# Kernel tuning notes

Hardware: AMD Instinct MI355X
Metric: run time of the kernel (lower is better)

Reference implementation:

```python
import jax, jax.numpy as jnp
import numpy as np

B, S, D, H = 8, 1024, 1024, 16
DH = D // H
EPS = 1e-5


def _layernorm(x):
    # elementwise_affine=False LayerNorm, eps=1e-5
    m = jnp.mean(x, axis=-1, keepdims=True)
    v = jnp.var(x, axis=-1, keepdims=True)
    return (x - m) * jax.lax.rsqrt(v + EPS)


def setup_inputs() -> dict:
    key = jax.random.key(0)
    ks = jax.random.split(key, 11)
    s = 0.02
    return {
        "x": jax.random.normal(ks[0], (B, S, D), jnp.float32),
        "y": jax.random.normal(ks[1], (B, 1, D), jnp.float32),
        "w_adaln": jax.random.normal(ks[2], (6 * D, D), jnp.float32) * s,
        "b_adaln": jnp.zeros((6 * D,), jnp.float32),
        "w_qkv": jax.random.normal(ks[3], (3 * D, D), jnp.float32) * s,
        "w_proj": jax.random.normal(ks[4], (D, D), jnp.float32) * s,
        "b_proj": jnp.zeros((D,), jnp.float32),
        "w_fc1": jax.random.normal(ks[5], (4 * D, D), jnp.float32) * s,
        "b_fc1": jnp.zeros((4 * D,), jnp.float32),
        "w_fc2": jax.random.normal(ks[6], (D, 4 * D), jnp.float32) * s,
        "b_fc2": jnp.zeros((D,), jnp.float32),
    }


def reference(x, y, w_adaln, b_adaln, w_qkv, w_proj, b_proj, w_fc1, b_fc1, w_fc2, b_fc2):
    # adaLN-Zero modulation params from conditioning y: SiLU -> Linear -> 6 chunks
    mods = jax.nn.silu(y) @ w_adaln.T + b_adaln          # [B,1,6D]
    sh_a, sc_a, g_a, sh_m, sc_m, g_m = jnp.split(mods, 6, axis=-1)

    # --- attention branch ---
    xm = _layernorm(x) * (1.0 + sc_a) + sh_a             # modulate
    qkv = xm @ w_qkv.T                                   # [B,S,3D] (qkv_bias=False)
    q, k, v = [t.reshape(B, S, H, DH).transpose(0, 2, 1, 3) for t in jnp.split(qkv, 3, axis=-1)]
    scale = 1.0 / np.sqrt(DH)
    scores = jnp.einsum("bhqd,bhkd->bhqk", q, k) * scale  # unfused MATH-backend sdpa
    attn = jax.nn.softmax(scores, axis=-1)
    o = jnp.einsum("bhqk,bhkd->bhqd", attn, v)
    o = o.transpose(0, 2, 1, 3).reshape(B, S, D)
    o = o @ w_proj.T + b_proj
    x = x + g_a * o                                      # gated residual

    # --- MLP branch ---
    xm = _layernorm(x) * (1.0 + sc_m) + sh_m
    h = jax.nn.gelu(xm @ w_fc1.T + b_fc1, approximate=True)  # GELU(tanh)
    h = h @ w_fc2.T + b_fc2
    return x + g_m * h
```

## Files before the change

### kernel.cpp

```cpp
#include <hip/hip_runtime.h>

typedef __bf16 bf16;
typedef __attribute__((ext_vector_type(8))) __bf16 bf16x8;
typedef __attribute__((ext_vector_type(4))) __bf16 bf16x4;
typedef __attribute__((ext_vector_type(2))) __bf16 bf16x2;
typedef __attribute__((ext_vector_type(4))) float f32x4;

#define MFMA16(a, b, c) __builtin_amdgcn_mfma_f32_16x16x32_bf16((a), (b), (c), 0, 0, 0)

__device__ __forceinline__ float clampf(float v, float c) {
    return fminf(fmaxf(v, -c), c);
}

__device__ __forceinline__ void gload16(const void* g, void* l) {
    __builtin_amdgcn_global_load_lds((const __attribute__((address_space(1))) void*)g,
                                     (__attribute__((address_space(3))) void*)l, 16, 0, 0);
}

__launch_bounds__(256)
__global__ void cvt_kernel(const float* __restrict__ src, bf16* __restrict__ dst, int n4)
{
    int i = blockIdx.x * 256 + threadIdx.x;
    if (i < n4) {
        float4 v = ((const float4*)src)[i];
        bf16x4 o;
        o[0] = (bf16)v.x; o[1] = (bf16)v.y; o[2] = (bf16)v.z; o[3] = (bf16)v.w;
        ((bf16x4*)dst)[i] = o;
    }
}

__launch_bounds__(256)
__global__ void adaln_kernel(const float* __restrict__ y, const float* __restrict__ w,
                             const float* __restrict__ bias, float* __restrict__ mods)
{
    const int b = blockIdx.y;
    const int n = blockIdx.x * 256 + threadIdx.x;
    __shared__ float sy[1024];
    for (int i = threadIdx.x; i < 1024; i += 256) {
        float t = y[b * 1024 + i];
        sy[i] = t / (1.f + __expf(-t));
    }
    __syncthreads();
    const float* wr = w + (size_t)n * 1024;
    float acc = 0.f;
    for (int k = 0; k < 1024; k += 4) {
        float4 wv = *(const float4*)(wr + k);
        acc += sy[k] * wv.x + sy[k + 1] * wv.y + sy[k + 2] * wv.z + sy[k + 3] * wv.w;
    }
    mods[b * 6144 + n] = clampf(acc + bias[n], 64.f);
}

__launch_bounds__(256)
__global__ void ln_mod_kernel(const float* __restrict__ xin, const float* __restrict__ mods,
                              int shOff, int scOff, bf16* __restrict__ out)
{
    const int row = blockIdx.x;
    const int b = row >> 10;
    const int tid = threadIdx.x;
    const int wave = tid >> 6, lane = tid & 63;

    const float4 x4 = *((const float4*)xin + (size_t)row * 256 + tid);
    float v[4] = {x4.x, x4.y, x4.z, x4.w};

    float s = v[0] + v[1] + v[2] + v[3];
    float ss = v[0]*v[0] + v[1]*v[1] + v[2]*v[2] + v[3]*v[3];
#pragma unroll
    for (int o = 32; o > 0; o >>= 1) {
        s  += __shfl_xor(s, o, 64);
        ss += __shfl_xor(ss, o, 64);
    }
    __shared__ float red[8];
    if (lane == 0) { red[wave] = s; red[4 + wave] = ss; }
    __syncthreads();
    s  = red[0] + red[1] + red[2] + red[3];
    ss = red[4] + red[5] + red[6] + red[7];
    const float mean = s * (1.f / 1024.f);
    const float var  = ss * (1.f / 1024.f) - mean * mean;
    const float rstd = rsqrtf(fmaxf(var, 0.f) + 1e-5f);

    const float* mb = mods + b * 6144;
    bf16x4 o4;
#pragma unroll
    for (int j = 0; j < 4; ++j) {
        int c = tid * 4 + j;
        o4[j] = (bf16)clampf(((v[j] - mean) * rstd) * (1.f + mb[scOff + c]) + mb[shOff + c], 64.f);
    }
    *((bf16x4*)out + (size_t)row * 256 + tid) = o4;
}

template <int EPI>
__launch_bounds__(256)
__global__ void gemm_fast(const bf16* __restrict__ A, const bf16* __restrict__ W,
                          const float* __restrict__ bias, const float* __restrict__ mods,
                          int gateOff, const float* __restrict__ resid,
                          float* __restrict__ of, bf16* __restrict__ ob,
                          int N, int K, int nN, float clampV)
{
    __shared__ __align__(16) bf16 As[128 * 32];
    __shared__ __align__(16) bf16 Bs[128 * 32];

    const int tid = threadIdx.x;
    const int wave = tid >> 6, lane = tid & 63, quad = lane >> 4, l16 = lane & 15;
    const int wrow = wave >> 1, wcol = wave & 1;

    const int bid = blockIdx.x;
    const int c = bid & 7;
    const int j = bid >> 3;
    const int tileM = (c * 8 + j / nN) * 128;
    const int tileN = (j % nN) * 128;

    const bf16* Ag = A + (size_t)(tileM + (tid >> 2)) * K + (tid & 3) * 8;
    const bf16* Wg = W + (size_t)(tileN + (tid >> 2)) * K + (tid & 3) * 8;
    bf16* AsW = As + wave * 512;
    bf16* BsW = Bs + wave * 512;
    const size_t rowStep = (size_t)64 * K;

    f32x4 acc[4][4] = {};

    for (int k0 = 0; k0 < K; k0 += 32) {
        gload16(Ag + k0, AsW);
        gload16(Ag + rowStep + k0, AsW + 2048);
        gload16(Wg + k0, BsW);
        gload16(Wg + rowStep + k0, BsW + 2048);
        __syncthreads();

        bf16x8 af[4], bfr[4];
#pragma unroll
        for (int mt = 0; mt < 4; ++mt)
            af[mt] = *(const bf16x8*)&As[(wrow * 64 + mt * 16 + l16) * 32 + quad * 8];
#pragma unroll
        for (int nt = 0; nt < 4; ++nt)
            bfr[nt] = *(const bf16x8*)&Bs[(wcol * 64 + nt * 16 + l16) * 32 + quad * 8];
#pragma unroll
        for (int mt = 0; mt < 4; ++mt)
#pragma unroll
            for (int nt = 0; nt < 4; ++nt)
                acc[mt][nt] = MFMA16(af[mt], bfr[nt], acc[mt][nt]);
        __syncthreads();
    }

#pragma unroll
    for (int mt = 0; mt < 4; ++mt) {
#pragma unroll
        for (int nt = 0; nt < 4; ++nt) {
            const int col = tileN + wcol * 64 + nt * 16 + l16;
#pragma unroll
            for (int i = 0; i < 4; ++i) {
                const int row = tileM + wrow * 64 + mt * 16 + quad * 4 + i;
                float v = acc[mt][nt][i];
                if (EPI != 0) v += bias[col];
                if (EPI == 0) {
                    ob[(size_t)row * N + col] = (bf16)clampf(v, clampV);
                } else if (EPI == 1) {
                    const int bb = row >> 10;
                    const float g = mods[bb * 6144 + gateOff + col];
                    of[(size_t)row * N + col] =
                        clampf(resid[(size_t)row * N + col] + g * v, clampV);
                } else {
                    const float e = __expf(1.5957691216f * (v + 0.044715f * v * v * v));
                    const float t = 1.f - 2.f / (e + 1.f);
                    ob[(size_t)row * N + col] = (bf16)clampf(0.5f * v * (1.f + t), clampV);
                }
            }
        }
    }
}

template <int EPI>
__launch_bounds__(256)
__global__ void gemm_bt(const bf16* __restrict__ A, const float* __restrict__ W,
                        const float* __restrict__ bias, const float* __restrict__ mods,
                        int gateOff, const float* __restrict__ resid,
                        float* __restrict__ of, bf16* __restrict__ ob,
                        int M, int N, int K, float clampV)
{
    constexpr int LDT = 40;
    __shared__ bf16 As[128 * LDT];
    __shared__ bf16 Bs[128 * LDT];

    const int tid = threadIdx.x;
    const int wave = tid >> 6, lane = tid & 63, quad = lane >> 4, l16 = lane & 15;
    const int wrow = wave >> 1, wcol = wave & 1;
    const int tileM = blockIdx.y * 128, tileN = blockIdx.x * 128;
    const int sr = tid >> 2;
    const int sk = (tid & 3) * 8;

    const bf16*  Ag = A + (size_t)(tileM + sr) * K + sk;
    const float* Wg = W + (size_t)(tileN + sr) * K + sk;

    f32x4 acc[4][4] = {};

    for (int k0 = 0; k0 < K; k0 += 32) {
        bf16x8 a0 = *(const bf16x8*)(Ag + k0);
        bf16x8 a1 = *(const bf16x8*)(Ag + (size_t)64 * K + k0);
        float4 w0a = *(const float4*)(Wg + k0);
        float4 w0b = *(const float4*)(Wg + k0 + 4);
        float4 w1a = *(const float4*)(Wg + (size_t)64 * K + k0);
        float4 w1b = *(const float4*)(Wg + (size_t)64 * K + k0 + 4);
        bf16x8 b0, b1;
        b0[0] = (bf16)w0a.x; b0[1] = (bf16)w0a.y; b0[2] = (bf16)w0a.z; b0[3] = (bf16)w0a.w;
        b0[4] = (bf16)w0b.x; b0[5] = (bf16)w0b.y; b0[6] = (bf16)w0b.z; b0[7] = (bf16)w0b.w;
        b1[0] = (bf16)w1a.x; b1[1] = (bf16)w1a.y; b1[2] = (bf16)w1a.z; b1[3] = (bf16)w1a.w;
        b1[4] = (bf16)w1b.x; b1[5] = (bf16)w1b.y; b1[6] = (bf16)w1b.z; b1[7] = (bf16)w1b.w;
        *(bf16x8*)&As[sr * LDT + sk] = a0;
        *(bf16x8*)&As[(sr + 64) * LDT + sk] = a1;
        *(bf16x8*)&Bs[sr * LDT + sk] = b0;
        *(bf16x8*)&Bs[(sr + 64) * LDT + sk] = b1;
        __syncthreads();

        bf16x8 af[4], bfr[4];
#pragma unroll
        for (int mt = 0; mt < 4; ++mt)
            af[mt] = *(const bf16x8*)&As[(wrow * 64 + mt * 16 + l16) * LDT + quad * 8];
#pragma unroll
        for (int nt = 0; nt < 4; ++nt)
            bfr[nt] = *(const bf16x8*)&Bs[(wcol * 64 + nt * 16 + l16) * LDT + quad * 8];
#pragma unroll
        for (int mt = 0; mt < 4; ++mt)
#pragma unroll
            for (int nt = 0; nt < 4; ++nt)
                acc[mt][nt] = MFMA16(af[mt], bfr[nt], acc[mt][nt]);
        __syncthreads();
    }

#pragma unroll
    for (int mt = 0; mt < 4; ++mt) {
#pragma unroll
        for (int nt = 0; nt < 4; ++nt) {
            const int col = tileN + wcol * 64 + nt * 16 + l16;
#pragma unroll
            for (int i = 0; i < 4; ++i) {
                const int row = tileM + wrow * 64 + mt * 16 + quad * 4 + i;
                float v = acc[mt][nt][i];
                if (EPI != 0) v += bias[col];
                if (EPI == 0) {
                    ob[(size_t)row * N + col] = (bf16)clampf(v, clampV);
                } else if (EPI == 1) {
                    const int bb = row >> 10;
                    const float g = mods[bb * 6144 + gateOff + col];
                    of[(size_t)row * N + col] =
                        clampf(resid[(size_t)row * N + col] + g * v, clampV);
                } else {
                    const float e = __expf(1.5957691216f * (v + 0.044715f * v * v * v));
                    const float t = 1.f - 2.f / (e + 1.f);
                    ob[(size_t)row * N + col] = (bf16)clampf(0.5f * v * (1.f + t), clampV);
                }
            }
        }
    }
}

__launch_bounds__(256)
__global__ void attn_kernel(const bf16* __restrict__ qkv, bf16* __restrict__ o)
{
    const int bid = blockIdx.x;
    const int qt = bid >> 7;
    const int b  = (bid >> 4) & 7;
    const int h  = bid & 15;
    const int tid = threadIdx.x;
    const int wave = tid >> 6, lane = tid & 63, quad = lane >> 4, l16 = lane & 15;

    __shared__ bf16 Kl[64 * 72];
    __shared__ bf16 Vt[64 * 72];
    __shared__ bf16 Pl[4][32 * 72];

    const size_t basebs = (size_t)b * 1024 * 3072;
    const int qbase = qt * 128 + wave * 32;

    bf16x8 qf[2][2];
#pragma unroll
    for (int mt = 0; mt < 2; ++mt)
#pragma unroll
        for (int kk = 0; kk < 2; ++kk) {
            const int row = qbase + mt * 16 + l16;
            const int dh = kk * 32 + quad * 8;
            qf[mt][kk] = *(const bf16x8*)(qkv + basebs + (size_t)row * 3072 + h * 64 + dh);
        }

    const int kr = tid >> 2, kc = (tid & 3) * 16;
    const int vp = tid >> 3, vc = (tid & 7) * 8;
    const bf16* Kg = qkv + basebs + (size_t)kr * 3072 + 1024 + h * 64 + kc;
    const bf16* Vg = qkv + basebs + (size_t)(2 * vp) * 3072 + 2048 + h * 64 + vc;
    const size_t ktStep = (size_t)64 * 3072;

    bf16x8 k0 = *(const bf16x8*)Kg;
    bf16x8 k1 = *(const bf16x8*)(Kg + 8);
    bf16x8 v0 = *(const bf16x8*)Vg;
    bf16x8 v1 = *(const bf16x8*)(Vg + 3072);

    f32x4 oacc[2][4] = {};
    float lsum[2][4] = {};

    for (int kt = 0; kt < 16; ++kt) {
        *(bf16x8*)&Kl[kr * 72 + kc] = k0;
        *(bf16x8*)&Kl[kr * 72 + kc + 8] = k1;
#pragma unroll
        for (int j = 0; j < 8; ++j) {
            bf16x2 pr; pr[0] = v0[j]; pr[1] = v1[j];
            *(bf16x2*)&Vt[(vc + j) * 72 + 2 * vp] = pr;
        }
        __syncthreads();

        const size_t noff = (size_t)(kt < 15 ? kt + 1 : 15) * ktStep;
        k0 = *(const bf16x8*)(Kg + noff);
        k1 = *(const bf16x8*)(Kg + noff + 8);
        v0 = *(const bf16x8*)(Vg + noff);
        v1 = *(const bf16x8*)(Vg + noff + 3072);

        f32x4 s[2][4] = {};
#pragma unroll
        for (int kk = 0; kk < 2; ++kk)
#pragma unroll
            for (int nt = 0; nt < 4; ++nt) {
                bf16x8 kf = *(const bf16x8*)&Kl[(nt * 16 + l16) * 72 + kk * 32 + quad * 8];
#pragma unroll
                for (int mt = 0; mt < 2; ++mt)
                    s[mt][nt] = MFMA16(qf[mt][kk], kf, s[mt][nt]);
            }

#pragma unroll
        for (int mt = 0; mt < 2; ++mt)
#pragma unroll
            for (int nt = 0; nt < 4; ++nt)
#pragma unroll
                for (int i = 0; i < 4; ++i) {
                    float p = exp2f(fminf(s[mt][nt][i] * 0.18033688f, 43.f));
                    Pl[wave][(mt * 16 + quad * 4 + i) * 72 + nt * 16 + l16] = (bf16)p;
                    lsum[mt][i] += p;
                }

#pragma unroll
        for (int kk = 0; kk < 2; ++kk) {
            bf16x8 pf[2];
#pragma unroll
            for (int mt = 0; mt < 2; ++mt)
                pf[mt] = *(const bf16x8*)&Pl[wave][(mt * 16 + l16) * 72 + kk * 32 + quad * 8];
#pragma unroll
            for (int nt = 0; nt < 4; ++nt) {
                bf16x8 vf = *(const bf16x8*)&Vt[(nt * 16 + l16) * 72 + kk * 32 + quad * 8];
#pragma unroll
                for (int mt = 0; mt < 2; ++mt)
                    oacc[mt][nt] = MFMA16(pf[mt], vf, oacc[mt][nt]);
            }
        }
        __syncthreads();
    }

    bf16* ob = o + (size_t)b * 1024 * 1024 + h * 64;
#pragma unroll
    for (int mt = 0; mt < 2; ++mt)
#pragma unroll
        for (int i = 0; i < 4; ++i) {
            float l = lsum[mt][i];
#pragma unroll
            for (int off = 1; off < 16; off <<= 1) l += __shfl_xor(l, off, 64);
            const float inv = 1.f / fmaxf(l, 1e-20f);
            const int row = qbase + mt * 16 + quad * 4 + i;
#pragma unroll
            for (int nt = 0; nt < 4; ++nt)
                ob[(size_t)row * 1024 + nt * 16 + l16] = (bf16)clampf(oacc[mt][nt][i] * inv, 16.f);
        }
}

extern "C" void kernel_launch(void* const* d_in, const int* in_sizes, int n_in,
                              void* d_out, int out_size, void* d_ws, size_t ws_size,
                              hipStream_t stream)
{
    const float* x       = (const float*)d_in[0];
    const float* y       = (const float*)d_in[1];
    const float* w_adaln = (const float*)d_in[2];
    const float* b_adaln = (const float*)d_in[3];
    const float* w_qkv   = (const float*)d_in[4];
    const float* w_proj  = (const float*)d_in[5];
    const float* b_proj  = (const float*)d_in[6];
    const float* w_fc1   = (const float*)d_in[7];
    const float* b_fc1   = (const float*)d_in[8];
    const float* w_fc2   = (const float*)d_in[9];
    const float* b_fc2   = (const float*)d_in[10];
    float* out = (float*)d_out;

    char* ws = (char*)d_ws;
    float* mods = (float*)ws;
    bf16* bufA  = (bf16*)(ws + (1ull << 18));
    bf16* bufH  = (bf16*)(ws + (1ull << 18) + (1ull << 24));
    size_t off = (1ull << 18) + (1ull << 24) + (1ull << 26);
    bf16* wb_qkv  = (bf16*)(ws + off);               off += 6ull << 20;
    bf16* wb_proj = (bf16*)(ws + off);               off += 2ull << 20;
    bf16* wb_fc1  = (bf16*)(ws + off);               off += 8ull << 20;
    bf16* wb_fc2  = (bf16*)(ws + off);               off += 8ull << 20;
    const bool fast = ws_size >= off;

    adaln_kernel<<<dim3(24, 8), 256, 0, stream>>>(y, w_adaln, b_adaln, mods);
    ln_mod_kernel<<<8192, 256, 0, stream>>>(x, mods, 0, 1024, bufA);

    if (fast) {
        cvt_kernel<<<(3072 * 256 + 255) / 256, 256, 0, stream>>>(w_qkv, wb_qkv, 3072 * 256);
        cvt_kernel<<<(1024 * 256 + 255) / 256, 256, 0, stream>>>(w_proj, wb_proj, 1024 * 256);
        cvt_kernel<<<(4096 * 256 + 255) / 256, 256, 0, stream>>>(w_fc1, wb_fc1, 4096 * 256);
        cvt_kernel<<<(4096 * 256 + 255) / 256, 256, 0, stream>>>(w_fc2, wb_fc2, 4096 * 256);

        gemm_fast<0><<<24 * 64, 256, 0, stream>>>(bufA, wb_qkv, nullptr, nullptr, 0,
                                                  nullptr, nullptr, bufH, 3072, 1024, 24, 64.f);
        attn_kernel<<<1024, 256, 0, stream>>>(bufH, bufA);
        gemm_fast<1><<<8 * 64, 256, 0, stream>>>(bufA, wb_proj, b_proj, mods, 2048,
                                                 x, out, nullptr, 1024, 1024, 8, 64.f);
        ln_mod_kernel<<<8192, 256, 0, stream>>>(out, mods, 3072, 4096, bufA);
        gemm_fast<2><<<32 * 64, 256, 0, stream>>>(bufA, wb_fc1, b_fc1, nullptr, 0,
                                                  nullptr, nullptr, bufH, 4096, 1024, 32, 64.f);
        gemm_fast<1><<<8 * 64, 256, 0, stream>>>(bufH, wb_fc2, b_fc2, mods, 5120,
                                                 out, out, nullptr, 1024, 4096, 8, 64.f);
    } else {
        gemm_bt<0><<<dim3(24, 64), 256, 0, stream>>>(bufA, w_qkv, nullptr, nullptr, 0,
                                                     nullptr, nullptr, bufH, 8192, 3072, 1024, 64.f);
        attn_kernel<<<1024, 256, 0, stream>>>(bufH, bufA);
        gemm_bt<1><<<dim3(8, 64), 256, 0, stream>>>(bufA, w_proj, b_proj, mods, 2048,
                                                    x, out, nullptr, 8192, 1024, 1024, 64.f);
        ln_mod_kernel<<<8192, 256, 0, stream>>>(out, mods, 3072, 4096, bufA);
        gemm_bt<2><<<dim3(32, 64), 256, 0, stream>>>(bufA, w_fc1, b_fc1, nullptr, 0,
                                                     nullptr, nullptr, bufH, 8192, 4096, 1024, 64.f);
        gemm_bt<1><<<dim3(8, 64), 256, 0, stream>>>(bufH, w_fc2, b_fc2, mods, 5120,
                                                    out, out, nullptr, 8192, 1024, 4096, 64.f);
    }
}
```

Before: 617.5 us.

## Replace bf16 GEMMs with 256x256 double-buffered 8-wave ping-pong kernel

```diff
diff --git a/kernel.cpp b/kernel.cpp
--- a/kernel.cpp
+++ b/kernel.cpp
@@ -89,48 +89,218 @@
 }
 
 template <int EPI>
+__launch_bounds__(512, 2)
+__global__ void gemm_8ph(const bf16* __restrict__ A, const bf16* __restrict__ W,
+                         const float* __restrict__ bias, const float* __restrict__ mods,
+                         int gateOff, const float* __restrict__ resid,
+                         float* __restrict__ of, bf16* __restrict__ ob,
+                         int N, int K, int nN, float clampV)
+{
+    __shared__ __align__(16) bf16 sm[2][2][2][8192];
+
+    const int tid = threadIdx.x;
+    const int wave = tid >> 6, lane = tid & 63, quad = lane >> 4, l16 = lane & 15;
+    const int wm = wave >> 2, wn = wave & 3;
+
+    const int cpx = gridDim.x >> 3;
+    const int wg = ((int)blockIdx.x & 7) * cpx + ((int)blockIdx.x >> 3);
+    const int tileM = (wg / nN) * 256;
+    const int tileN = (wg % nN) * 256;
+
+    const int p0 = tid * 16;
+    const int l0 = p0 ^ (((p0 >> 7) & 7) << 4);
+    const int srow = l0 >> 7;
+    const int scol = (l0 & 127) >> 1;
+    const bf16* Ag = A + (size_t)(tileM + srow) * K + scol;
+    const bf16* Wg = W + (size_t)(tileN + srow) * K + scol;
+    const size_t halfStep = (size_t)128 * K;
+    const size_t slotStep = (size_t)64 * K;
+
+    const int xorv = (l16 & 7) << 4;
+    const int cx0 = (quad * 16) ^ xorv;
+    const int cx1 = (64 + quad * 16) ^ xorv;
+    const int bofs = (wn & 1) * 64;
+
+    f32x4 acc[8][4] = {};
+    bf16x8 af[4][2], b0[2][2], b1[2][2];
+
+#define STAGE8(d, h, kt) do { \
+        const bf16* g_ = ((h) < 2 ? Ag : Wg) + (size_t)((h) & 1) * halfStep + (size_t)(kt) * 64; \
+        bf16* l_ = &sm[d][(h) >> 1][(h) & 1][wave * 512]; \
+        gload16(g_, l_); \
+        gload16(g_ + slotStep, l_ + 4096); \
+    } while (0)
+
+#define RD_AF8(d, mb) do { \
+        _Pragma("unroll") for (int m_ = 0; m_ < 4; ++m_) { \
+            const char* r_ = (const char*)&sm[d][0][wm][0] + ((mb) + m_ * 16 + l16) * 128; \
+            af[m_][0] = *(const bf16x8*)(r_ + cx0); \
+            af[m_][1] = *(const bf16x8*)(r_ + cx1); \
+        } \
+    } while (0)
+
+#define RD_B8(d, arr, nb) do { \
+        _Pragma("unroll") for (int n_ = 0; n_ < 2; ++n_) { \
+            const char* r_ = (const char*)&sm[d][1][wn >> 1][0] + (bofs + (nb) + n_ * 16 + l16) * 128; \
+            arr[n_][0] = *(const bf16x8*)(r_ + cx0); \
+            arr[n_][1] = *(const bf16x8*)(r_ + cx1); \
+        } \
+    } while (0)
+
+#define MM8(mb, arr, nb) do { \
+        __builtin_amdgcn_s_setprio(1); \
+        _Pragma("unroll") for (int m_ = 0; m_ < 4; ++m_) \
+        _Pragma("unroll") for (int n_ = 0; n_ < 2; ++n_) { \
+            acc[(mb) + m_][(nb) + n_] = MFMA16(af[m_][0], arr[n_][0], acc[(mb) + m_][(nb) + n_]); \
+            acc[(mb) + m_][(nb) + n_] = MFMA16(af[m_][1], arr[n_][1], acc[(mb) + m_][(nb) + n_]); \
+        } \
+        __builtin_amdgcn_s_setprio(0); \
+    } while (0)
+
+#define BARF() do { __builtin_amdgcn_s_barrier(); asm volatile("" ::: "memory"); } while (0)
+#define LGKM0() do { asm volatile("s_waitcnt lgkmcnt(0)" ::: "memory"); \
+                     __builtin_amdgcn_sched_barrier(0); } while (0)
+#define VMC2() do { asm volatile("s_waitcnt vmcnt(2)" ::: "memory"); \
+                    __builtin_amdgcn_sched_barrier(0); } while (0)
+
+    STAGE8(0, 0, 0); STAGE8(0, 1, 0); STAGE8(0, 2, 0); STAGE8(0, 3, 0);
+    STAGE8(1, 0, 1);
+    VMC2();
+    BARF();
+
+    const int nkt = K >> 6;
+    for (int t = 0; t < nkt; t += 2) {
+        const int t2 = (t + 2 < nkt) ? t + 2 : nkt - 1;
+        const int t3 = (t + 3 < nkt) ? t + 3 : nkt - 1;
+        RD_AF8(0, 0); RD_B8(0, b0, 0);
+        STAGE8(1, 1, t + 1);
+        BARF(); LGKM0();
+        MM8(0, b0, 0);
+        BARF();
+        RD_B8(0, b1, 32);
+        STAGE8(1, 2, t + 1);
+        BARF(); LGKM0();
+        MM8(0, b1, 2);
+        BARF();
+        RD_AF8(0, 64);
+        STAGE8(1, 3, t + 1);
+        BARF(); LGKM0();
+        MM8(4, b1, 2);
+        BARF();
+        STAGE8(0, 0, t2);
+        BARF();
+        MM8(4, b0, 0);
+        VMC2();
+        BARF();
+        RD_AF8(1, 0); RD_B8(1, b0, 0);
+        STAGE8(0, 1, t2);
+        BARF(); LGKM0();
+        MM8(0, b0, 0);
+        BARF();
+        RD_B8(1, b1, 32);
+        STAGE8(0, 2, t2);
+        BARF(); LGKM0();
+        MM8(0, b1, 2);
+        BARF();
+        RD_AF8(1, 64);
+        STAGE8(0, 3, t2);
+        BARF(); LGKM0();
+        MM8(4, b1, 2);
+        BARF();
+        STAGE8(1, 0, t3);
+        BARF();
+        MM8(4, b0, 0);
+        VMC2();
+        BARF();
+    }
+    asm volatile("s_waitcnt vmcnt(0)" ::: "memory");
+
+#undef STAGE8
+#undef RD_AF8
+#undef RD_B8
+#undef MM8
+#undef BARF
+#undef LGKM0
+#undef VMC2
+
+    const int rowB = tileM + wm * 128 + quad * 4;
+    const int colB = tileN + wn * 64 + l16;
+#pragma unroll
+    for (int mt = 0; mt < 8; ++mt) {
+#pragma unroll
+        for (int nt = 0; nt < 4; ++nt) {
+            const int col = colB + nt * 16;
+#pragma unroll
+            for (int i = 0; i < 4; ++i) {
+                const int row = rowB + mt * 16 + i;
+                float v = acc[mt][nt][i];
+                if (EPI != 0) v += bias[col];
+                if (EPI == 0) {
+                    ob[(size_t)row * N + col] = (bf16)clampf(v, clampV);
+                } else if (EPI == 1) {
+                    const int bb = row >> 10;
+                    const float g = mods[bb * 6144 + gateOff + col];
+                    of[(size_t)row * N + col] =
+                        clampf(resid[(size_t)row * N + col] + g * v, clampV);
+                } else {
+                    const float e = __expf(1.5957691216f * (v + 0.044715f * v * v * v));
+                    const float tt = 1.f - 2.f / (e + 1.f);
+                    ob[(size_t)row * N + col] = (bf16)clampf(0.5f * v * (1.f + tt), clampV);
+                }
+            }
+        }
+    }
+}
+
+template <int EPI>
 __launch_bounds__(256)
-__global__ void gemm_fast(const bf16* __restrict__ A, const bf16* __restrict__ W,
-                          const float* __restrict__ bias, const float* __restrict__ mods,
-                          int gateOff, const float* __restrict__ resid,
-                          float* __restrict__ of, bf16* __restrict__ ob,
-                          int N, int K, int nN, float clampV)
-{
-    __shared__ __align__(16) bf16 As[128 * 32];
-    __shared__ __align__(16) bf16 Bs[128 * 32];
+__global__ void gemm_bt(const bf16* __restrict__ A, const float* __restrict__ W,
+                        const float* __restrict__ bias, const float* __restrict__ mods,
+                        int gateOff, const float* __restrict__ resid,
+                        float* __restrict__ of, bf16* __restrict__ ob,
+                        int M, int N, int K, float clampV)
+{
+    constexpr int LDT = 40;
+    __shared__ bf16 As[128 * LDT];
+    __shared__ bf16 Bs[128 * LDT];
 
     const int tid = threadIdx.x;
     const int wave = tid >> 6, lane = tid & 63, quad = lane >> 4, l16 = lane & 15;
     const int wrow = wave >> 1, wcol = wave & 1;
-
-    const int bid = blockIdx.x;
-    const int c = bid & 7;
-    const int j = bid >> 3;
-    const int tileM = (c * 8 + j / nN) * 128;
-    const int tileN = (j % nN) * 128;
-
-    const bf16* Ag = A + (size_t)(tileM + (tid >> 2)) * K + (tid & 3) * 8;
-    const bf16* Wg = W + (size_t)(tileN + (tid >> 2)) * K + (tid & 3) * 8;
-    bf16* AsW = As + wave * 512;
-    bf16* BsW = Bs + wave * 512;
-    const size_t rowStep = (size_t)64 * K;
+    const int tileM = blockIdx.y * 128, tileN = blockIdx.x * 128;
+    const int sr = tid >> 2;
+    const int sk = (tid & 3) * 8;
+
+    const bf16*  Ag = A + (size_t)(tileM + sr) * K + sk;
+    const float* Wg = W + (size_t)(tileN + sr) * K + sk;
 
     f32x4 acc[4][4] = {};
 
     for (int k0 = 0; k0 < K; k0 += 32) {
-        gload16(Ag + k0, AsW);
-        gload16(Ag + rowStep + k0, AsW + 2048);
-        gload16(Wg + k0, BsW);
-        gload16(Wg + rowStep + k0, BsW + 2048);
+        bf16x8 a0 = *(const bf16x8*)(Ag + k0);
+        bf16x8 a1 = *(const bf16x8*)(Ag + (size_t)64 * K + k0);
+        float4 w0a = *(const float4*)(Wg + k0);
+        float4 w0b = *(const float4*)(Wg + k0 + 4);
+        float4 w1a = *(const float4*)(Wg + (size_t)64 * K + k0);
+        float4 w1b = *(const float4*)(Wg + (size_t)64 * K + k0 + 4);
+        bf16x8 b0, b1;
+        b0[0] = (bf16)w0a.x; b0[1] = (bf16)w0a.y; b0[2] = (bf16)w0a.z; b0[3] = (bf16)w0a.w;
+        b0[4] = (bf16)w0b.x; b0[5] = (bf16)w0b.y; b0[6] = (bf16)w0b.z; b0[7] = (bf16)w0b.w;
+        b1[0] = (bf16)w1a.x; b1[1] = (bf16)w1a.y; b1[2] = (bf16)w1a.z; b1[3] = (bf16)w1a.w;
+        b1[4] = (bf16)w1b.x; b1[5] = (bf16)w1b.y; b1[6] = (bf16)w1b.z; b1[7] = (bf16)w1b.w;
+        *(bf16x8*)&As[sr * LDT + sk] = a0;
+        *(bf16x8*)&As[(sr + 64) * LDT + sk] = a1;
+        *(bf16x8*)&Bs[sr * LDT + sk] = b0;
+        *(bf16x8*)&Bs[(sr + 64) * LDT + sk] = b1;
         __syncthreads();
 
         bf16x8 af[4], bfr[4];
 #pragma unroll
         for (int mt = 0; mt < 4; ++mt)
-            af[mt] = *(const bf16x8*)&As[(wrow * 64 + mt * 16 + l16) * 32 + quad * 8];
+            af[mt] = *(const bf16x8*)&As[(wrow * 64 + mt * 16 + l16) * LDT + quad * 8];
 #pragma unroll
         for (int nt = 0; nt < 4; ++nt)
-            bfr[nt] = *(const bf16x8*)&Bs[(wcol * 64 + nt * 16 + l16) * 32 + quad * 8];
+            bfr[nt] = *(const bf16x8*)&Bs[(wcol * 64 + nt * 16 + l16) * LDT + quad * 8];
 #pragma unroll
         for (int mt = 0; mt < 4; ++mt)
 #pragma unroll
@@ -166,90 +336,6 @@
     }
 }
 
-template <int EPI>
-__launch_bounds__(256)
-__global__ void gemm_bt(const bf16* __restrict__ A, const float* __restrict__ W,
-                        const float* __restrict__ bias, const float* __restrict__ mods,
-                        int gateOff, const float* __restrict__ resid,
-                        float* __restrict__ of, bf16* __restrict__ ob,
-                        int M, int N, int K, float clampV)
-{
-    constexpr int LDT = 40;
-    __shared__ bf16 As[128 * LDT];
-    __shared__ bf16 Bs[128 * LDT];
-
-    const int tid = threadIdx.x;
-    const int wave = tid >> 6, lane = tid & 63, quad = lane >> 4, l16 = lane & 15;
-    const int wrow = wave >> 1, wcol = wave & 1;
-    const int tileM = blockIdx.y * 128, tileN = blockIdx.x * 128;
-    const int sr = tid >> 2;
-    const int sk = (tid & 3) * 8;
-
-    const bf16*  Ag = A + (size_t)(tileM + sr) * K + sk;
-    const float* Wg = W + (size_t)(tileN + sr) * K + sk;
-
-    f32x4 acc[4][4] = {};
-
-    for (int k0 = 0; k0 < K; k0 += 32) {
-        bf16x8 a0 = *(const bf16x8*)(Ag + k0);
-        bf16x8 a1 = *(const bf16x8*)(Ag + (size_t)64 * K + k0);
-        float4 w0a = *(const float4*)(Wg + k0);
-        float4 w0b = *(const float4*)(Wg + k0 + 4);
-        float4 w1a = *(const float4*)(Wg + (size_t)64 * K + k0);
-        float4 w1b = *(const float4*)(Wg + (size_t)64 * K + k0 + 4);
-        bf16x8 b0, b1;
-        b0[0] = (bf16)w0a.x; b0[1] = (bf16)w0a.y; b0[2] = (bf16)w0a.z; b0[3] = (bf16)w0a.w;
-        b0[4] = (bf16)w0b.x; b0[5] = (bf16)w0b.y; b0[6] = (bf16)w0b.z; b0[7] = (bf16)w0b.w;
-        b1[0] = (bf16)w1a.x; b1[1] = (bf16)w1a.y; b1[2] = (bf16)w1a.z; b1[3] = (bf16)w1a.w;
-        b1[4] = (bf16)w1b.x; b1[5] = (bf16)w1b.y; b1[6] = (bf16)w1b.z; b1[7] = (bf16)w1b.w;
-        *(bf16x8*)&As[sr * LDT + sk] = a0;
-        *(bf16x8*)&As[(sr + 64) * LDT + sk] = a1;
-        *(bf16x8*)&Bs[sr * LDT + sk] = b0;
-        *(bf16x8*)&Bs[(sr + 64) * LDT + sk] = b1;
-        __syncthreads();
-
-        bf16x8 af[4], bfr[4];
-#pragma unroll
-        for (int mt = 0; mt < 4; ++mt)
-            af[mt] = *(const bf16x8*)&As[(wrow * 64 + mt * 16 + l16) * LDT + quad * 8];
-#pragma unroll
-        for (int nt = 0; nt < 4; ++nt)
-            bfr[nt] = *(const bf16x8*)&Bs[(wcol * 64 + nt * 16 + l16) * LDT + quad * 8];
-#pragma unroll
-        for (int mt = 0; mt < 4; ++mt)
-#pragma unroll
-            for (int nt = 0; nt < 4; ++nt)
-                acc[mt][nt] = MFMA16(af[mt], bfr[nt], acc[mt][nt]);
-        __syncthreads();
-    }
-
-#pragma unroll
-    for (int mt = 0; mt < 4; ++mt) {
-#pragma unroll
-        for (int nt = 0; nt < 4; ++nt) {
-            const int col = tileN + wcol * 64 + nt * 16 + l16;
-#pragma unroll
-            for (int i = 0; i < 4; ++i) {
-                const int row = tileM + wrow * 64 + mt * 16 + quad * 4 + i;
-                float v = acc[mt][nt][i];
-                if (EPI != 0) v += bias[col];
-                if (EPI == 0) {
-                    ob[(size_t)row * N + col] = (bf16)clampf(v, clampV);
-                } else if (EPI == 1) {
-                    const int bb = row >> 10;
-                    const float g = mods[bb * 6144 + gateOff + col];
-                    of[(size_t)row * N + col] =
-                        clampf(resid[(size_t)row * N + col] + g * v, clampV);
-                } else {
-                    const float e = __expf(1.5957691216f * (v + 0.044715f * v * v * v));
-                    const float t = 1.f - 2.f / (e + 1.f);
-                    ob[(size_t)row * N + col] = (bf16)clampf(0.5f * v * (1.f + t), clampV);
-                }
-            }
-        }
-    }
-}
-
 __launch_bounds__(256)
 __global__ void attn_kernel(const bf16* __restrict__ qkv, bf16* __restrict__ o)
 {
@@ -399,16 +485,16 @@
         cvt_kernel<<<(4096 * 256 + 255) / 256, 256, 0, stream>>>(w_fc1, wb_fc1, 4096 * 256);
         cvt_kernel<<<(4096 * 256 + 255) / 256, 256, 0, stream>>>(w_fc2, wb_fc2, 4096 * 256);
 
-        gemm_fast<0><<<24 * 64, 256, 0, stream>>>(bufA, wb_qkv, nullptr, nullptr, 0,
-                                                  nullptr, nullptr, bufH, 3072, 1024, 24, 64.f);
+        gemm_8ph<0><<<32 * 12, 512, 0, stream>>>(bufA, wb_qkv, nullptr, nullptr, 0,
+                                                 nullptr, nullptr, bufH, 3072, 1024, 12, 64.f);
         attn_kernel<<<1024, 256, 0, stream>>>(bufH, bufA);
-        gemm_fast<1><<<8 * 64, 256, 0, stream>>>(bufA, wb_proj, b_proj, mods, 2048,
-                                                 x, out, nullptr, 1024, 1024, 8, 64.f);
+        gemm_8ph<1><<<32 * 4, 512, 0, stream>>>(bufA, wb_proj, b_proj, mods, 2048,
+                                                x, out, nullptr, 1024, 1024, 4, 64.f);
         ln_mod_kernel<<<8192, 256, 0, stream>>>(out, mods, 3072, 4096, bufA);
-        gemm_fast<2><<<32 * 64, 256, 0, stream>>>(bufA, wb_fc1, b_fc1, nullptr, 0,
-                                                  nullptr, nullptr, bufH, 4096, 1024, 32, 64.f);
-        gemm_fast<1><<<8 * 64, 256, 0, stream>>>(bufH, wb_fc2, b_fc2, mods, 5120,
-                                                 out, out, nullptr, 1024, 4096, 8, 64.f);
+        gemm_8ph<2><<<32 * 16, 512, 0, stream>>>(bufA, wb_fc1, b_fc1, nullptr, 0,
+                                                 nullptr, nullptr, bufH, 4096, 1024, 16, 64.f);
+        gemm_8ph<1><<<32 * 4, 512, 0, stream>>>(bufH, wb_fc2, b_fc2, mods, 5120,
+                                                out, out, nullptr, 1024, 4096, 4, 64.f);
     } else {
         gemm_bt<0><<<dim3(24, 64), 256, 0, stream>>>(bufA, w_qkv, nullptr, nullptr, 0,
                                                      nullptr, nullptr, bufH, 8192, 3072, 1024, 64.f);
```

Result: faster. 570.2 us (-7.7%).

## Replace bf16 GEMMs with 256x128-tile triple-buffered LDS-pipelined kernel

Applied to the files above, without the earlier changes.

```diff
diff --git a/kernel.cpp b/kernel.cpp
--- a/kernel.cpp
+++ b/kernel.cpp
@@ -89,48 +89,185 @@
 }
 
 template <int EPI>
+__launch_bounds__(512, 2)
+__global__ void gemm_np(const bf16* __restrict__ A, const bf16* __restrict__ W,
+                        const float* __restrict__ bias, const float* __restrict__ mods,
+                        int gateOff, const float* __restrict__ resid,
+                        float* __restrict__ of, bf16* __restrict__ ob,
+                        int N, int K, int nN, float clampV)
+{
+    __shared__ __align__(16) bf16 sm[3][3][8192];
+
+    const int tid = threadIdx.x;
+    const int wave = tid >> 6, lane = tid & 63, quad = lane >> 4, l16 = lane & 15;
+    const int wm = wave >> 1, wn = wave & 1;
+
+    const int cpx = gridDim.x >> 3;
+    const int wg = ((int)blockIdx.x & 7) * cpx + ((int)blockIdx.x >> 3);
+    const int tileM = (wg / nN) * 256;
+    const int tileN = (wg % nN) * 128;
+
+    const int p0 = tid * 16;
+    const int l0 = p0 ^ (((p0 >> 7) & 7) << 4);
+    const int srow = l0 >> 7;
+    const int scol = (l0 & 127) >> 1;
+    const bf16* Ag  = A + (size_t)(tileM + srow) * K + scol;
+    const bf16* Ag2 = Ag + (size_t)128 * K;
+    const bf16* Wg  = W + (size_t)(tileN + srow) * K + scol;
+    const size_t slotStep = (size_t)64 * K;
+
+    const int xorv = (l16 & 7) << 4;
+    const int cx0 = (quad * 16) ^ xorv;
+    const int cx1 = (64 + quad * 16) ^ xorv;
+
+    f32x4 acc[4][4] = {};
+    bf16x8 af[4], bfr[4];
+
+#define SPASS(r2, reg, src, p, ts) \
+    gload16((src) + (size_t)(p) * slotStep + (size_t)(ts) * 64, \
+            &sm[r2][reg][(p) * 4096 + wave * 512])
+
+#define RDNP(r, cx) do { \
+        _Pragma("unroll") for (int q_ = 0; q_ < 4; ++q_) { \
+            af[q_]  = *(const bf16x8*)((const char*)&sm[r][wm >> 1][0] + \
+                        (((wm & 1) * 64 + q_ * 16 + l16) * 128) + (cx)); \
+            bfr[q_] = *(const bf16x8*)((const char*)&sm[r][2][0] + \
+                        ((wn * 64 + q_ * 16 + l16) * 128) + (cx)); \
+        } \
+    } while (0)
+
+#define MMNP() do { \
+        __builtin_amdgcn_s_setprio(1); \
+        _Pragma("unroll") for (int m_ = 0; m_ < 4; ++m_) \
+        _Pragma("unroll") for (int n_ = 0; n_ < 4; ++n_) \
+            acc[m_][n_] = MFMA16(af[m_], bfr[n_], acc[m_][n_]); \
+        __builtin_amdgcn_s_setprio(0); \
+    } while (0)
+
+#define BARF() do { __builtin_amdgcn_s_barrier(); asm volatile("" ::: "memory"); } while (0)
+#define LGKM0() do { asm volatile("s_waitcnt lgkmcnt(0)" ::: "memory"); \
+                     __builtin_amdgcn_sched_barrier(0); } while (0)
+#define VMC6() do { asm volatile("s_waitcnt vmcnt(6)" ::: "memory"); \
+                    __builtin_amdgcn_sched_barrier(0); } while (0)
+
+#define KTILE(r, r2, T) do { \
+        const int ts_ = ((T) + 2 < nkt) ? (T) + 2 : nkt - 1; \
+         \
+        RDNP(r, cx0); \
+        SPASS(r2, 0, Ag, 0, ts_); SPASS(r2, 0, Ag, 1, ts_); SPASS(r2, 1, Ag2, 0, ts_); \
+        BARF(); LGKM0(); \
+        MMNP(); \
+        BARF(); \
+         \
+        RDNP(r, cx1); \
+        SPASS(r2, 1, Ag2, 1, ts_); SPASS(r2, 2, Wg, 0, ts_); SPASS(r2, 2, Wg, 1, ts_); \
+        BARF(); LGKM0(); \
+        MMNP(); \
+        VMC6(); \
+        BARF(); \
+    } while (0)
+
+    const int nkt = K >> 6;
+    SPASS(0, 0, Ag, 0, 0); SPASS(0, 0, Ag, 1, 0); SPASS(0, 1, Ag2, 0, 0);
+    SPASS(0, 1, Ag2, 1, 0); SPASS(0, 2, Wg, 0, 0); SPASS(0, 2, Wg, 1, 0);
+    SPASS(1, 0, Ag, 0, 1); SPASS(1, 0, Ag, 1, 1); SPASS(1, 1, Ag2, 0, 1);
+    SPASS(1, 1, Ag2, 1, 1); SPASS(1, 2, Wg, 0, 1); SPASS(1, 2, Wg, 1, 1);
+    VMC6();
+    BARF();
+
+    for (int t = 0; t < nkt; t += 3) {
+        KTILE(0, 2, t);
+        if (t + 1 < nkt) KTILE(1, 0, t + 1);
+        if (t + 2 < nkt) KTILE(2, 1, t + 2);
+    }
+    asm volatile("s_waitcnt vmcnt(0)" ::: "memory");
+
+#undef SPASS
+#undef RDNP
+#undef MMNP
+#undef BARF
+#undef LGKM0
+#undef VMC6
+#undef KTILE
+
+    const int rowB = tileM + wm * 64 + quad * 4;
+    const int colB = tileN + wn * 64 + l16;
+#pragma unroll
+    for (int mt = 0; mt < 4; ++mt) {
+#pragma unroll
+        for (int nt = 0; nt < 4; ++nt) {
+            const int col = colB + nt * 16;
+#pragma unroll
+            for (int i = 0; i < 4; ++i) {
+                const int row = rowB + mt * 16 + i;
+                float v = acc[mt][nt][i];
+                if (EPI != 0) v += bias[col];
+                if (EPI == 0) {
+                    ob[(size_t)row * N + col] = (bf16)clampf(v, clampV);
+                } else if (EPI == 1) {
+                    const int bb = row >> 10;
+                    const float g = mods[bb * 6144 + gateOff + col];
+                    of[(size_t)row * N + col] =
+                        clampf(resid[(size_t)row * N + col] + g * v, clampV);
+                } else {
+                    const float e = __expf(1.5957691216f * (v + 0.044715f * v * v * v));
+                    const float tt = 1.f - 2.f / (e + 1.f);
+                    ob[(size_t)row * N + col] = (bf16)clampf(0.5f * v * (1.f + tt), clampV);
+                }
+            }
+        }
+    }
+}
+
+template <int EPI>
 __launch_bounds__(256)
-__global__ void gemm_fast(const bf16* __restrict__ A, const bf16* __restrict__ W,
-                          const float* __restrict__ bias, const float* __restrict__ mods,
-                          int gateOff, const float* __restrict__ resid,
-                          float* __restrict__ of, bf16* __restrict__ ob,
-                          int N, int K, int nN, float clampV)
-{
-    __shared__ __align__(16) bf16 As[128 * 32];
-    __shared__ __align__(16) bf16 Bs[128 * 32];
+__global__ void gemm_bt(const bf16* __restrict__ A, const float* __restrict__ W,
+                        const float* __restrict__ bias, const float* __restrict__ mods,
+                        int gateOff, const float* __restrict__ resid,
+                        float* __restrict__ of, bf16* __restrict__ ob,
+                        int M, int N, int K, float clampV)
+{
+    constexpr int LDT = 40;
+    __shared__ bf16 As[128 * LDT];
+    __shared__ bf16 Bs[128 * LDT];
 
     const int tid = threadIdx.x;
     const int wave = tid >> 6, lane = tid & 63, quad = lane >> 4, l16 = lane & 15;
     const int wrow = wave >> 1, wcol = wave & 1;
-
-    const int bid = blockIdx.x;
-    const int c = bid & 7;
-    const int j = bid >> 3;
-    const int tileM = (c * 8 + j / nN) * 128;
-    const int tileN = (j % nN) * 128;
-
-    const bf16* Ag = A + (size_t)(tileM + (tid >> 2)) * K + (tid & 3) * 8;
-    const bf16* Wg = W + (size_t)(tileN + (tid >> 2)) * K + (tid & 3) * 8;
-    bf16* AsW = As + wave * 512;
-    bf16* BsW = Bs + wave * 512;
-    const size_t rowStep = (size_t)64 * K;
+    const int tileM = blockIdx.y * 128, tileN = blockIdx.x * 128;
+    const int sr = tid >> 2;
+    const int sk = (tid & 3) * 8;
+
+    const bf16*  Ag = A + (size_t)(tileM + sr) * K + sk;
+    const float* Wg = W + (size_t)(tileN + sr) * K + sk;
 
     f32x4 acc[4][4] = {};
 
     for (int k0 = 0; k0 < K; k0 += 32) {
-        gload16(Ag + k0, AsW);
-        gload16(Ag + rowStep + k0, AsW + 2048);
-        gload16(Wg + k0, BsW);
-        gload16(Wg + rowStep + k0, BsW + 2048);
+        bf16x8 a0 = *(const bf16x8*)(Ag + k0);
+        bf16x8 a1 = *(const bf16x8*)(Ag + (size_t)64 * K + k0);
+        float4 w0a = *(const float4*)(Wg + k0);
+        float4 w0b = *(const float4*)(Wg + k0 + 4);
+        float4 w1a = *(const float4*)(Wg + (size_t)64 * K + k0);
+        float4 w1b = *(const float4*)(Wg + (size_t)64 * K + k0 + 4);
+        bf16x8 b0, b1;
+        b0[0] = (bf16)w0a.x; b0[1] = (bf16)w0a.y; b0[2] = (bf16)w0a.z; b0[3] = (bf16)w0a.w;
+        b0[4] = (bf16)w0b.x; b0[5] = (bf16)w0b.y; b0[6] = (bf16)w0b.z; b0[7] = (bf16)w0b.w;
+        b1[0] = (bf16)w1a.x; b1[1] = (bf16)w1a.y; b1[2] = (bf16)w1a.z; b1[3] = (bf16)w1a.w;
+        b1[4] = (bf16)w1b.x; b1[5] = (bf16)w1b.y; b1[6] = (bf16)w1b.z; b1[7] = (bf16)w1b.w;
+        *(bf16x8*)&As[sr * LDT + sk] = a0;
+        *(bf16x8*)&As[(sr + 64) * LDT + sk] = a1;
+        *(bf16x8*)&Bs[sr * LDT + sk] = b0;
+        *(bf16x8*)&Bs[(sr + 64) * LDT + sk] = b1;
         __syncthreads();
 
         bf16x8 af[4], bfr[4];
 #pragma unroll
         for (int mt = 0; mt < 4; ++mt)
-            af[mt] = *(const bf16x8*)&As[(wrow * 64 + mt * 16 + l16) * 32 + quad * 8];
+            af[mt] = *(const bf16x8*)&As[(wrow * 64 + mt * 16 + l16) * LDT + quad * 8];
 #pragma unroll
         for (int nt = 0; nt < 4; ++nt)
-            bfr[nt] = *(const bf16x8*)&Bs[(wcol * 64 + nt * 16 + l16) * 32 + quad * 8];
+            bfr[nt] = *(const bf16x8*)&Bs[(wcol * 64 + nt * 16 + l16) * LDT + quad * 8];
 #pragma unroll
         for (int mt = 0; mt < 4; ++mt)
 #pragma unroll
@@ -166,90 +303,6 @@
     }
 }
 
-template <int EPI>
-__launch_bounds__(256)
-__global__ void gemm_bt(const bf16* __restrict__ A, const float* __restrict__ W,
-                        const float* __restrict__ bias, const float* __restrict__ mods,
-                        int gateOff, const float* __restrict__ resid,
-                        float* __restrict__ of, bf16* __restrict__ ob,
-                        int M, int N, int K, float clampV)
-{
-    constexpr int LDT = 40;
-    __shared__ bf16 As[128 * LDT];
-    __shared__ bf16 Bs[128 * LDT];
-
-    const int tid = threadIdx.x;
-    const int wave = tid >> 6, lane = tid & 63, quad = lane >> 4, l16 = lane & 15;
-    const int wrow = wave >> 1, wcol = wave & 1;
-    const int tileM = blockIdx.y * 128, tileN = blockIdx.x * 128;
-    const int sr = tid >> 2;
-    const int sk = (tid & 3) * 8;
-
-    const bf16*  Ag = A + (size_t)(tileM + sr) * K + sk;
-    const float* Wg = W + (size_t)(tileN + sr) * K + sk;
-
-    f32x4 acc[4][4] = {};
-
-    for (int k0 = 0; k0 < K; k0 += 32) {
-        bf16x8 a0 = *(const bf16x8*)(Ag + k0);
-        bf16x8 a1 = *(const bf16x8*)(Ag + (size_t)64 * K + k0);
-        float4 w0a = *(const float4*)(Wg + k0);
-        float4 w0b = *(const float4*)(Wg + k0 + 4);
-        float4 w1a = *(const float4*)(Wg + (size_t)64 * K + k0);
-        float4 w1b = *(const float4*)(Wg + (size_t)64 * K + k0 + 4);
-        bf16x8 b0, b1;
-        b0[0] = (bf16)w0a.x; b0[1] = (bf16)w0a.y; b0[2] = (bf16)w0a.z; b0[3] = (bf16)w0a.w;
-        b0[4] = (bf16)w0b.x; b0[5] = (bf16)w0b.y; b0[6] = (bf16)w0b.z; b0[7] = (bf16)w0b.w;
-        b1[0] = (bf16)w1a.x; b1[1] = (bf16)w1a.y; b1[2] = (bf16)w1a.z; b1[3] = (bf16)w1a.w;
-        b1[4] = (bf16)w1b.x; b1[5] = (bf16)w1b.y; b1[6] = (bf16)w1b.z; b1[7] = (bf16)w1b.w;
-        *(bf16x8*)&As[sr * LDT + sk] = a0;
-        *(bf16x8*)&As[(sr + 64) * LDT + sk] = a1;
-        *(bf16x8*)&Bs[sr * LDT + sk] = b0;
-        *(bf16x8*)&Bs[(sr + 64) * LDT + sk] = b1;
-        __syncthreads();
-
-        bf16x8 af[4], bfr[4];
-#pragma unroll
-        for (int mt = 0; mt < 4; ++mt)
-            af[mt] = *(const bf16x8*)&As[(wrow * 64 + mt * 16 + l16) * LDT + quad * 8];
-#pragma unroll
-        for (int nt = 0; nt < 4; ++nt)
-            bfr[nt] = *(const bf16x8*)&Bs[(wcol * 64 + nt * 16 + l16) * LDT + quad * 8];
-#pragma unroll
-        for (int mt = 0; mt < 4; ++mt)
-#pragma unroll
-            for (int nt = 0; nt < 4; ++nt)
-                acc[mt][nt] = MFMA16(af[mt], bfr[nt], acc[mt][nt]);
-        __syncthreads();
-    }
-
-#pragma unroll
-    for (int mt = 0; mt < 4; ++mt) {
-#pragma unroll
-        for (int nt = 0; nt < 4; ++nt) {
-            const int col = tileN + wcol * 64 + nt * 16 + l16;
-#pragma unroll
-            for (int i = 0; i < 4; ++i) {
-                const int row = tileM + wrow * 64 + mt * 16 + quad * 4 + i;
-                float v = acc[mt][nt][i];
-                if (EPI != 0) v += bias[col];
-                if (EPI == 0) {
-                    ob[(size_t)row * N + col] = (bf16)clampf(v, clampV);
-                } else if (EPI == 1) {
-                    const int bb = row >> 10;
-                    const float g = mods[bb * 6144 + gateOff + col];
-                    of[(size_t)row * N + col] =
-                        clampf(resid[(size_t)row * N + col] + g * v, clampV);
-                } else {
-                    const float e = __expf(1.5957691216f * (v + 0.044715f * v * v * v));
-                    const float t = 1.f - 2.f / (e + 1.f);
-                    ob[(size_t)row * N + col] = (bf16)clampf(0.5f * v * (1.f + t), clampV);
-                }
-            }
-        }
-    }
-}
-
 __launch_bounds__(256)
 __global__ void attn_kernel(const bf16* __restrict__ qkv, bf16* __restrict__ o)
 {
@@ -399,16 +452,16 @@
         cvt_kernel<<<(4096 * 256 + 255) / 256, 256, 0, stream>>>(w_fc1, wb_fc1, 4096 * 256);
         cvt_kernel<<<(4096 * 256 + 255) / 256, 256, 0, stream>>>(w_fc2, wb_fc2, 4096 * 256);
 
-        gemm_fast<0><<<24 * 64, 256, 0, stream>>>(bufA, wb_qkv, nullptr, nullptr, 0,
-                                                  nullptr, nullptr, bufH, 3072, 1024, 24, 64.f);
+        gemm_np<0><<<768, 512, 0, stream>>>(bufA, wb_qkv, nullptr, nullptr, 0,
+                                            nullptr, nullptr, bufH, 3072, 1024, 24, 64.f);
         attn_kernel<<<1024, 256, 0, stream>>>(bufH, bufA);
-        gemm_fast<1><<<8 * 64, 256, 0, stream>>>(bufA, wb_proj, b_proj, mods, 2048,
-                                                 x, out, nullptr, 1024, 1024, 8, 64.f);
+        gemm_np<1><<<256, 512, 0, stream>>>(bufA, wb_proj, b_proj, mods, 2048,
+                                            x, out, nullptr, 1024, 1024, 8, 64.f);
         ln_mod_kernel<<<8192, 256, 0, stream>>>(out, mods, 3072, 4096, bufA);
-        gemm_fast<2><<<32 * 64, 256, 0, stream>>>(bufA, wb_fc1, b_fc1, nullptr, 0,
-                                                  nullptr, nullptr, bufH, 4096, 1024, 32, 64.f);
-        gemm_fast<1><<<8 * 64, 256, 0, stream>>>(bufH, wb_fc2, b_fc2, mods, 5120,
-                                                 out, out, nullptr, 1024, 4096, 8, 64.f);
+        gemm_np<2><<<1024, 512, 0, stream>>>(bufA, wb_fc1, b_fc1, nullptr, 0,
+                                             nullptr, nullptr, bufH, 4096, 1024, 32, 64.f);
+        gemm_np<1><<<256, 512, 0, stream>>>(bufH, wb_fc2, b_fc2, mods, 5120,
+                                            out, out, nullptr, 1024, 4096, 8, 64.f);
     } else {
         gemm_bt<0><<<dim3(24, 64), 256, 0, stream>>>(bufA, w_qkv, nullptr, nullptr, 0,
                                                      nullptr, nullptr, bufH, 8192, 3072, 1024, 64.f);
```

Result: faster. 544.9 us (-11.8%).
